# Optimization experiments

Hardware: AMD Instinct MI355X
Metric: run time of the kernel (lower is better)

The kernel has to match this reference:

```python
import jax, jax.numpy as jnp
import numpy as np

N = 100000      # nodes
E = 1600000     # edges
G = 8           # graphs in batch
H = 128         # hidden_dim
CNN = 768
MORPH = 6
NC = 5
EPS = 1e-5      # BatchNorm eps


def setup_inputs() -> dict:
    key = jax.random.key(0)
    ks = jax.random.split(key, 32)
    D = CNN + MORPH

    def w(k, shape, fan_in):
        # kaiming_normal_ (relu): std = sqrt(2/fan_in)
        return jax.random.normal(k, shape, jnp.float32) * np.sqrt(2.0 / fan_in)

    inp = {
        "cnn_features": jax.random.normal(ks[0], (N, CNN), jnp.float32),
        "morph_features": jax.random.normal(ks[1], (N, MORPH), jnp.float32),
        "cell_edge_index": jax.random.randint(ks[2], (2, E), 0, N, jnp.int32),
        "batch": jnp.sort(jax.random.randint(ks[3], (N,), 0, G, jnp.int32)),
        # GCN layers (weights stored [in, out])
        "gcn1_w": w(ks[4], (D, H), D), "gcn1_b": jnp.zeros((H,), jnp.float32),
        "gcn2_w": w(ks[5], (H, H), H), "gcn2_b": jnp.zeros((H,), jnp.float32),
        "gcn3_w": w(ks[6], (H, H), H), "gcn3_b": jnp.zeros((H,), jnp.float32),
        # BatchNorm affine params (eval mode, running_mean=0 running_var=1)
        "bn1_g": jnp.ones((H,), jnp.float32), "bn1_b": jnp.zeros((H,), jnp.float32),
        "bn2_g": jnp.ones((H,), jnp.float32), "bn2_b": jnp.zeros((H,), jnp.float32),
        "bn3_g": jnp.ones((H,), jnp.float32), "bn3_b": jnp.zeros((H,), jnp.float32),
        # attention gate: Linear(H,H) -> tanh -> Linear(H,1)
        "att_w1": w(ks[7], (H, H), H), "att_b1": jnp.zeros((H,), jnp.float32),
        "att_w2": w(ks[8], (H, 1), H), "att_b2": jnp.zeros((1,), jnp.float32),
        # classifier MLP
        "cls_w1": w(ks[9], (H, 2 * H), H), "cls_b1": jnp.zeros((2 * H,), jnp.float32),
        "cbn1_g": jnp.ones((2 * H,), jnp.float32), "cbn1_b": jnp.zeros((2 * H,), jnp.float32),
        "cls_w2": w(ks[10], (2 * H, H), 2 * H), "cls_b2": jnp.zeros((H,), jnp.float32),
        "cbn2_g": jnp.ones((H,), jnp.float32), "cbn2_b": jnp.zeros((H,), jnp.float32),
        "cls_w3": w(ks[11], (H, NC), H), "cls_b3": jnp.zeros((NC,), jnp.float32),
    }
    return inp


def _bn_eval(x, gamma, beta):
    # BatchNorm1d eval: running_mean=0, running_var=1
    return x * (gamma / np.sqrt(1.0 + EPS)) + beta


def _gcn(x, w, b, src, dst, dinv):
    h = x @ w                                   # [N, out]
    norm = dinv[src] * dinv[dst]                # [E]
    msg = h[src] * norm[:, None]                # [E, out]
    agg = jax.ops.segment_sum(msg, dst, num_segments=N)
    agg = agg + h * (dinv * dinv)[:, None]      # self-loop contribution
    return agg + b


def _forward(cnn_features, morph_features,
             gcn1_w, gcn1_b, gcn2_w, gcn2_b, gcn3_w, gcn3_b,
             bn1_g, bn1_b, bn2_g, bn2_b, bn3_g, bn3_b,
             att_w1, att_b1, att_w2, att_b2,
             cls_w1, cls_b1, cbn1_g, cbn1_b,
             cls_w2, cls_b2, cbn2_g, cbn2_b,
             cls_w3, cls_b3,
             cell_edge_index, batch):
    x = jnp.concatenate([cnn_features, morph_features], axis=1)  # [N, 774]
    src, dst = cell_edge_index[0], cell_edge_index[1]
    # symmetric GCN normalization with self-loops: deg = in-degree + 1
    deg = jax.ops.segment_sum(jnp.ones((E,), x.dtype), dst, num_segments=N) + 1.0
    dinv = jax.lax.rsqrt(deg)

    x1 = jax.nn.relu(_bn_eval(_gcn(x, gcn1_w, gcn1_b, src, dst, dinv), bn1_g, bn1_b))
    x2 = jax.nn.relu(_bn_eval(_gcn(x1, gcn2_w, gcn2_b, src, dst, dinv), bn2_g, bn2_b))
    x3 = jax.nn.relu(_bn_eval(_gcn(x2, gcn3_w, gcn3_b, src, dst, dinv), bn3_g, bn3_b))
    x_out = x1 + x2 + x3                                        # [N, H]

    # GlobalAttention pooling: segment softmax over per-graph nodes
    gate = jnp.tanh(x_out @ att_w1 + att_b1) @ att_w2 + att_b2  # [N, 1]
    gate = gate[:, 0]
    gmax = jax.ops.segment_max(gate, batch, num_segments=G)
    a = jnp.exp(gate - gmax[batch])
    denom = jax.ops.segment_sum(a, batch, num_segments=G)
    alpha = a / denom[batch]
    pooled = jax.ops.segment_sum(alpha[:, None] * x_out, batch, num_segments=G)  # [G, H]

    # classifier (dropout off, BN eval)
    h = jax.nn.relu(_bn_eval(pooled @ cls_w1 + cls_b1, cbn1_g, cbn1_b))
    h = jax.nn.relu(_bn_eval(h @ cls_w2 + cls_b2, cbn2_g, cbn2_b))
    return h @ cls_w3 + cls_b3                                  # [G, NC]


def reference(cnn_features, morph_features, cell_edge_index, batch,
              gcn1_w, gcn1_b, gcn2_w, gcn2_b, gcn3_w, gcn3_b,
              bn1_g, bn1_b, bn2_g, bn2_b, bn3_g, bn3_b,
              att_w1, att_b1, att_w2, att_b2,
              cls_w1, cls_b1, cbn1_g, cbn1_b,
              cls_w2, cls_b2, cbn2_g, cbn2_b,
              cls_w3, cls_b3):
    return _forward(cnn_features, morph_features,
                    gcn1_w, gcn1_b, gcn2_w, gcn2_b, gcn3_w, gcn3_b,
                    bn1_g, bn1_b, bn2_g, bn2_b, bn3_g, bn3_b,
                    att_w1, att_b1, att_w2, att_b2,
                    cls_w1, cls_b1, cbn1_g, cbn1_b,
                    cls_w2, cls_b2, cbn2_g, cbn2_b,
                    cls_w3, cls_b3,
                    cell_edge_index, batch)
```

## Files before the change

kernel.cpp:

```cpp
#include <hip/hip_runtime.h>
#include <hip/hip_bf16.h>

#define EPSV 1e-5f

typedef short short8v __attribute__((ext_vector_type(8)));
typedef float f32x4 __attribute__((ext_vector_type(4)));

__device__ __forceinline__ unsigned short f2bf(float f){
  unsigned u = __float_as_uint(f);
  unsigned r = u + 0x7fffu + ((u >> 16) & 1u);
  return (unsigned short)(r >> 16);
}
__device__ __forceinline__ unsigned pk2bf(float x, float y){
  return (unsigned)f2bf(x) | ((unsigned)f2bf(y) << 16);
}
__device__ __forceinline__ float bf2f(unsigned short s){
  return __uint_as_float(((unsigned)s) << 16);
}
__device__ __forceinline__ float bflo(unsigned u){ return __uint_as_float(u << 16); }
__device__ __forceinline__ float bfhi(unsigned u){ return __uint_as_float(u & 0xffff0000u); }

__global__ void hist_kernel(const int* __restrict__ dst, int* __restrict__ deg, int E){
  int i = blockIdx.x*256 + threadIdx.x;
  if (i < E) atomicAdd(&deg[dst[i]], 1);
}

__global__ void scan_partial(const int* __restrict__ deg, int* __restrict__ bsums, int N){
  __shared__ int sd[256];
  int t = threadIdx.x;
  int base = blockIdx.x*1024 + t*4;
  int s = 0;
  if (base+0 < N) s += deg[base+0];
  if (base+1 < N) s += deg[base+1];
  if (base+2 < N) s += deg[base+2];
  if (base+3 < N) s += deg[base+3];
  sd[t]=s; __syncthreads();
  for (int off=128; off>0; off>>=1){
    if (t<off) sd[t]+=sd[t+off];
    __syncthreads();
  }
  if (t==0) bsums[blockIdx.x]=sd[0];
}

__global__ void scan_bsums(int* bsums, int* row_start, int B, int N, int E){
  if (threadIdx.x==0 && blockIdx.x==0){
    int run=0;
    for (int b=0;b<B;b++){ int v=bsums[b]; bsums[b]=run; run+=v; }
    row_start[N]=E;
  }
}

__global__ void scan_final(const int* __restrict__ deg, const int* __restrict__ bsums,
                           int* __restrict__ row_start, int* __restrict__ cursor,
                           float* __restrict__ dinv, int N){
  __shared__ int sd[256];
  int t=threadIdx.x, b=blockIdx.x;
  int base=b*1024+t*4;
  int v0=0,v1=0,v2=0,v3=0;
  if (base+0<N) v0=deg[base+0];
  if (base+1<N) v1=deg[base+1];
  if (base+2<N) v2=deg[base+2];
  if (base+3<N) v3=deg[base+3];
  int s=v0+v1+v2+v3;
  sd[t]=s; __syncthreads();
  for (int off=1; off<256; off<<=1){
    int x = (t>=off)?sd[t-off]:0;
    __syncthreads();
    sd[t]+=x;
    __syncthreads();
  }
  int excl = sd[t]-s + bsums[b];
  int e0=excl, e1=excl+v0, e2=e1+v1, e3=e2+v2;
  if (base+0<N){ row_start[base+0]=e0; cursor[base+0]=e0; dinv[base+0]=rsqrtf((float)v0+1.0f); }
  if (base+1<N){ row_start[base+1]=e1; cursor[base+1]=e1; dinv[base+1]=rsqrtf((float)v1+1.0f); }
  if (base+2<N){ row_start[base+2]=e2; cursor[base+2]=e2; dinv[base+2]=rsqrtf((float)v2+1.0f); }
  if (base+3<N){ row_start[base+3]=e3; cursor[base+3]=e3; dinv[base+3]=rsqrtf((float)v3+1.0f); }
}

__global__ void scatter_kernel(const int* __restrict__ src, const int* __restrict__ dst,
                               int* __restrict__ cursor, int* __restrict__ csr_src, int E){
  int i = blockIdx.x*256 + threadIdx.x;
  if (i < E){
    int d = dst[i];
    int pos = atomicAdd(&cursor[d], 1);
    csr_src[pos] = src[i];
  }
}

__global__ void wsplit_kernel(const float* __restrict__ W, unsigned short* __restrict__ WT,
                              int D, int Dpad){
  int k = blockIdx.x*256 + threadIdx.x;
  int c = blockIdx.y;
  if (k >= Dpad) return;
  float v = (k < D) ? W[(size_t)k*128 + c] : 0.f;
  WT[(size_t)c*Dpad + k] = f2bf(v);
}

__global__ void wsplit_all(const float* __restrict__ W2, const float* __restrict__ W3,
                           const float* __restrict__ WA,
                           unsigned short* __restrict__ w2T, unsigned short* __restrict__ w3T,
                           unsigned short* __restrict__ aT_hi, unsigned short* __restrict__ aT_lo){
  int k = threadIdx.x;
  int c = blockIdx.y;
  int z = blockIdx.z;
  if (z == 0){
    w2T[c*128 + k] = f2bf(W2[(size_t)k*128 + c]);
  } else if (z == 1){
    w3T[c*128 + k] = f2bf(W3[(size_t)k*128 + c]);
  } else {
    float v = WA[(size_t)k*128 + c];
    unsigned short h = f2bf(v);
    aT_hi[c*128 + k] = h;
    aT_lo[c*128 + k] = f2bf(v - bf2f(h));
  }
}

#define LOADA(KC) { \
  const int gk0 = (KC) + akseg; \
  if ((Rst < N) && (gk0 + 32 <= Da)){ \
    const float4* p4 = (const float4*)(xa + (size_t)Rst*Da + gk0); \
    pa0=p4[0]; pa1=p4[1]; pa2=p4[2]; pa3=p4[3]; pa4=p4[4]; pa5=p4[5]; pa6=p4[6]; pa7=p4[7]; \
  } else { \
    float tmp[32]; \
    _Pragma("unroll") \
    for (int q=0;q<32;q++){ \
      int gk = gk0 + q; float x = 0.f; \
      if (Rst < N){ \
        if (gk < Da) x = xa[(size_t)Rst*Da + gk]; \
        else if (gk < D) x = xb[(size_t)Rst*Db + (gk - Da)]; \
      } \
      tmp[q]=x; } \
    pa0=*(float4*)&tmp[0];  pa1=*(float4*)&tmp[4];  pa2=*(float4*)&tmp[8];  pa3=*(float4*)&tmp[12]; \
    pa4=*(float4*)&tmp[16]; pa5=*(float4*)&tmp[20]; pa6=*(float4*)&tmp[24]; pa7=*(float4*)&tmp[28]; \
  } }

#define LOADW(KC) { \
  const unsigned short* ph = wrowp + (KC); \
  pw0=*(const uint4*)(ph); pw1=*(const uint4*)(ph+8); pw2=*(const uint4*)(ph+16); pw3=*(const uint4*)(ph+24); }

__global__ __launch_bounds__(256, 3) void gemm_mfma_kernel(
    const float* __restrict__ xa, const float* __restrict__ xb,
    const unsigned short* __restrict__ WT,
    unsigned short* __restrict__ outb, int N, int Da, int Db, int Dpad)
{
  __shared__ unsigned short Abf[128*64];
  __shared__ unsigned short Bbf[128*64];

  const int tid  = threadIdx.x;
  const int lane = tid & 63;
  const int wave = tid >> 6;
  const int lr   = lane & 15;
  const int kg   = lane >> 4;
  const int rowBase = blockIdx.x * 128;
  const int D = Da + Db;

  f32x4 acc[2][8];
  #pragma unroll
  for (int s=0;s<2;s++)
    #pragma unroll
    for (int c=0;c<8;c++){ acc[s][c][0]=0.f; acc[s][c][1]=0.f; acc[s][c][2]=0.f; acc[s][c][3]=0.f; }

  const int arow = tid >> 1;
  const int akseg = (tid & 1) * 32;
  const int Rst = rowBase + arow;
  const int abase = arow*128 + akseg*2;
  const int aswz  = (arow & 7) << 4;
  const unsigned short* wrowp = WT + (size_t)arow*Dpad + akseg;

  float4 pa0,pa1,pa2,pa3,pa4,pa5,pa6,pa7;
  uint4  pw0,pw1,pw2,pw3;

  LOADA(0)
  LOADW(0)

  for (int kc = 0; kc < Dpad; kc += 64){
    __syncthreads();
    {
      unsigned u[4];
      u[0]=pk2bf(pa0.x,pa0.y); u[1]=pk2bf(pa0.z,pa0.w); u[2]=pk2bf(pa1.x,pa1.y); u[3]=pk2bf(pa1.z,pa1.w);
      *(uint4*)((char*)Abf + ((abase+ 0)^aswz)) = *(const uint4*)u;
      u[0]=pk2bf(pa2.x,pa2.y); u[1]=pk2bf(pa2.z,pa2.w); u[2]=pk2bf(pa3.x,pa3.y); u[3]=pk2bf(pa3.z,pa3.w);
      *(uint4*)((char*)Abf + ((abase+16)^aswz)) = *(const uint4*)u;
      u[0]=pk2bf(pa4.x,pa4.y); u[1]=pk2bf(pa4.z,pa4.w); u[2]=pk2bf(pa5.x,pa5.y); u[3]=pk2bf(pa5.z,pa5.w);
      *(uint4*)((char*)Abf + ((abase+32)^aswz)) = *(const uint4*)u;
      u[0]=pk2bf(pa6.x,pa6.y); u[1]=pk2bf(pa6.z,pa6.w); u[2]=pk2bf(pa7.x,pa7.y); u[3]=pk2bf(pa7.z,pa7.w);
      *(uint4*)((char*)Abf + ((abase+48)^aswz)) = *(const uint4*)u;
      *(uint4*)((char*)Bbf + ((abase+ 0)^aswz)) = pw0;
      *(uint4*)((char*)Bbf + ((abase+16)^aswz)) = pw1;
      *(uint4*)((char*)Bbf + ((abase+32)^aswz)) = pw2;
      *(uint4*)((char*)Bbf + ((abase+48)^aswz)) = pw3;
    }
    __syncthreads();
    const int kn = kc + 64;
    if (kn < Dpad){
      LOADA(kn)
      LOADW(kn)
    }
    #pragma unroll
    for (int ks=0; ks<2; ks++){
      const int kb = ks*64 + kg*16;
      const int r0 = wave*32 + lr;
      const int r1 = r0 + 16;
      const int offA0 = (r0*128 + kb) ^ ((r0&7)<<4);
      const int offA1 = (r1*128 + kb) ^ ((r1&7)<<4);
      short8v a0 = *(const short8v*)((const char*)Abf + offA0);
      short8v a1 = *(const short8v*)((const char*)Abf + offA1);
      #pragma unroll
      for (int ct=0; ct<8; ct++){
        const int c = ct*16 + lr;
        const int offB = (c*128 + kb) ^ ((c&7)<<4);
        short8v b = *(const short8v*)((const char*)Bbf + offB);
        acc[0][ct] = __builtin_amdgcn_mfma_f32_16x16x32_bf16(a0, b, acc[0][ct], 0,0,0);
        acc[1][ct] = __builtin_amdgcn_mfma_f32_16x16x32_bf16(a1, b, acc[1][ct], 0,0,0);
      }
    }
  }
  const int wrow = rowBase + wave*32;
  #pragma unroll
  for (int strip=0; strip<2; strip++){
    #pragma unroll
    for (int ct=0; ct<8; ct++){
      #pragma unroll
      for (int i=0;i<4;i++){
        int R = wrow + strip*16 + kg*4 + i;
        int C = ct*16 + lr;
        if (R < N) outb[(size_t)R*128 + C] = f2bf(acc[strip][ct][i]);
      }
    }
  }
}

__global__ __launch_bounds__(256) void att_mfma_kernel(
    const float* __restrict__ xa,
    const unsigned short* __restrict__ WhiT, const unsigned short* __restrict__ WloT,
    const float* __restrict__ b1, const float* __restrict__ w2, const float* __restrict__ b2,
    const int* __restrict__ batch,
    float* __restrict__ aex, float* __restrict__ denom, int N)
{
  __shared__ unsigned short Ahi[128*64];
  __shared__ unsigned short Alo[128*64];
  __shared__ unsigned short Bhi[128*64];
  __shared__ unsigned short Blo[128*64];
  __shared__ float sden[8];

  const int tid  = threadIdx.x;
  const int lane = tid & 63;
  const int wave = tid >> 6;
  const int lr   = lane & 15;
  const int kg   = lane >> 4;
  const int rowBase = blockIdx.x * 128;

  if (tid < 8) sden[tid] = 0.f;

  f32x4 acc[2][8];
  #pragma unroll
  for (int s=0;s<2;s++)
    #pragma unroll
    for (int c=0;c<8;c++){ acc[s][c][0]=0.f; acc[s][c][1]=0.f; acc[s][c][2]=0.f; acc[s][c][3]=0.f; }

  const int arow = tid >> 1;
  const int akseg = (tid & 1) * 32;
  const int Rst = rowBase + arow;
  const int abase = arow*128 + akseg*2;
  const int aswz  = (arow & 7) << 4;

  for (int kc = 0; kc < 128; kc += 64){
    __syncthreads();
    {
      const int gk0 = kc + akseg;
      float4 v0={0,0,0,0},v1={0,0,0,0},v2={0,0,0,0},v3={0,0,0,0};
      float4 v4={0,0,0,0},v5={0,0,0,0},v6={0,0,0,0},v7={0,0,0,0};
      if (Rst < N){
        const float4* p4 = (const float4*)(xa + (size_t)Rst*128 + gk0);
        v0=p4[0]; v1=p4[1]; v2=p4[2]; v3=p4[3]; v4=p4[4]; v5=p4[5]; v6=p4[6]; v7=p4[7];
      }
#define STAGE_HL(VA, VB, SOFF) { \
      unsigned uh[4], ul[4]; \
      unsigned short h0=f2bf(VA.x), h1=f2bf(VA.y), h2=f2bf(VA.z), h3=f2bf(VA.w); \
      unsigned short h4=f2bf(VB.x), h5=f2bf(VB.y), h6=f2bf(VB.z), h7=f2bf(VB.w); \
      uh[0]=(unsigned)h0|((unsigned)h1<<16); uh[1]=(unsigned)h2|((unsigned)h3<<16); \
      uh[2]=(unsigned)h4|((unsigned)h5<<16); uh[3]=(unsigned)h6|((unsigned)h7<<16); \
      ul[0]=pk2bf(VA.x-bf2f(h0), VA.y-bf2f(h1)); ul[1]=pk2bf(VA.z-bf2f(h2), VA.w-bf2f(h3)); \
      ul[2]=pk2bf(VB.x-bf2f(h4), VB.y-bf2f(h5)); ul[3]=pk2bf(VB.z-bf2f(h6), VB.w-bf2f(h7)); \
      *(uint4*)((char*)Ahi + ((abase+(SOFF))^aswz)) = *(const uint4*)uh; \
      *(uint4*)((char*)Alo + ((abase+(SOFF))^aswz)) = *(const uint4*)ul; }
      STAGE_HL(v0, v1,  0)
      STAGE_HL(v2, v3, 16)
      STAGE_HL(v4, v5, 32)
      STAGE_HL(v6, v7, 48)
#undef STAGE_HL
    }
    {
      const unsigned short* ph = WhiT + (size_t)arow*128 + kc + akseg;
      const unsigned short* pl = WloT + (size_t)arow*128 + kc + akseg;
      *(uint4*)((char*)Bhi + ((abase+ 0)^aswz)) = *(const uint4*)(ph);
      *(uint4*)((char*)Bhi + ((abase+16)^aswz)) = *(const uint4*)(ph+8);
      *(uint4*)((char*)Bhi + ((abase+32)^aswz)) = *(const uint4*)(ph+16);
      *(uint4*)((char*)Bhi + ((abase+48)^aswz)) = *(const uint4*)(ph+24);
      *(uint4*)((char*)Blo + ((abase+ 0)^aswz)) = *(const uint4*)(pl);
      *(uint4*)((char*)Blo + ((abase+16)^aswz)) = *(const uint4*)(pl+8);
      *(uint4*)((char*)Blo + ((abase+32)^aswz)) = *(const uint4*)(pl+16);
      *(uint4*)((char*)Blo + ((abase+48)^aswz)) = *(const uint4*)(pl+24);
    }
    __syncthreads();
    #pragma unroll
    for (int ks=0; ks<2; ks++){
      const int kb = ks*64 + kg*16;
      const int r0 = wave*32 + lr;
      const int r1 = r0 + 16;
      const int offA0 = (r0*128 + kb) ^ ((r0&7)<<4);
      const int offA1 = (r1*128 + kb) ^ ((r1&7)<<4);
      short8v ah0 = *(const short8v*)((const char*)Ahi + offA0);
      short8v al0 = *(const short8v*)((const char*)Alo + offA0);
      short8v ah1 = *(const short8v*)((const char*)Ahi + offA1);
      short8v al1 = *(const short8v*)((const char*)Alo + offA1);
      #pragma unroll
      for (int ct=0; ct<8; ct++){
        const int c = ct*16 + lr;
        const int offB = (c*128 + kb) ^ ((c&7)<<4);
        short8v bh = *(const short8v*)((const char*)Bhi + offB);
        short8v bl = *(const short8v*)((const char*)Blo + offB);
        acc[0][ct] = __builtin_amdgcn_mfma_f32_16x16x32_bf16(ah0, bh, acc[0][ct], 0,0,0);
        acc[0][ct] = __builtin_amdgcn_mfma_f32_16x16x32_bf16(ah0, bl, acc[0][ct], 0,0,0);
        acc[0][ct] = __builtin_amdgcn_mfma_f32_16x16x32_bf16(al0, bh, acc[0][ct], 0,0,0);
        acc[1][ct] = __builtin_amdgcn_mfma_f32_16x16x32_bf16(ah1, bh, acc[1][ct], 0,0,0);
        acc[1][ct] = __builtin_amdgcn_mfma_f32_16x16x32_bf16(ah1, bl, acc[1][ct], 0,0,0);
        acc[1][ct] = __builtin_amdgcn_mfma_f32_16x16x32_bf16(al1, bh, acc[1][ct], 0,0,0);
      }
    }
  }
  float b1v[8], w2v[8];
  #pragma unroll
  for (int ct=0; ct<8; ct++){
    b1v[ct] = b1[ct*16 + lr];
    w2v[ct] = w2[ct*16 + lr];
  }
  const float bias2 = b2[0];
  const int wrow = rowBase + wave*32;
  #pragma unroll
  for (int strip=0; strip<2; strip++){
    #pragma unroll
    for (int i=0;i<4;i++){
      float p = 0.f;
      #pragma unroll
      for (int ct=0; ct<8; ct++){
        p += tanhf(acc[strip][ct][i] + b1v[ct]) * w2v[ct];
      }
      p += __shfl_xor(p, 1, 16);
      p += __shfl_xor(p, 2, 16);
      p += __shfl_xor(p, 4, 16);
      p += __shfl_xor(p, 8, 16);
      if (lr == 0){
        int R = wrow + strip*16 + kg*4 + i;
        if (R < N){
          float e = expf(p + bias2);
          aex[R] = e;
          atomicAdd(&sden[batch[R]], e);
        }
      }
    }
  }
  __syncthreads();
  if (tid < 8 && sden[tid] != 0.f) atomicAdd(&denom[tid], sden[tid]);
}

#define GFMA8(U, NJ) \
  a0=__builtin_fmaf(bflo(U.x),(NJ),a0); a1=__builtin_fmaf(bfhi(U.x),(NJ),a1); \
  a2=__builtin_fmaf(bflo(U.y),(NJ),a2); a3=__builtin_fmaf(bfhi(U.y),(NJ),a3); \
  a4=__builtin_fmaf(bflo(U.z),(NJ),a4); a5=__builtin_fmaf(bfhi(U.z),(NJ),a5); \
  a6=__builtin_fmaf(bflo(U.w),(NJ),a6); a7=__builtin_fmaf(bfhi(U.w),(NJ),a7);

__global__ __launch_bounds__(256) void gather_kernel(
    const unsigned short* __restrict__ hb, const float* __restrict__ dinv,
    const int* __restrict__ row_start, const int* __restrict__ csr_src,
    const float* __restrict__ bias, const float* __restrict__ bng, const float* __restrict__ bnb,
    const float* __restrict__ x1in, const float* __restrict__ x2in,
    float* __restrict__ out, int N, int mode)
{
  const int grp = (blockIdx.x * 256 + threadIdx.x) >> 4;
  const int sl  = threadIdx.x & 15;
  if (grp >= N) return;
  const int i = grp;
  const float di = dinv[i];
  const uint4* __restrict__ h4 = (const uint4*)hb;

  float a0,a1,a2,a3,a4,a5,a6,a7;
  {
    uint4 u = h4[(size_t)i*16 + sl];
    float w0 = di*di;
    a0=bflo(u.x)*w0; a1=bfhi(u.x)*w0; a2=bflo(u.y)*w0; a3=bfhi(u.y)*w0;
    a4=bflo(u.z)*w0; a5=bfhi(u.z)*w0; a6=bflo(u.w)*w0; a7=bfhi(u.w)*w0;
  }
  int base = row_start[i];
  const int s1 = row_start[i+1];
  while (base + 16 <= s1){
    int sv = csr_src[base + sl];
    float nv = dinv[sv]*di;
    #pragma unroll
    for (int j=0; j<16; j+=4){
      int sj0 = __shfl(sv, j,   16);
      int sj1 = __shfl(sv, j+1, 16);
      int sj2 = __shfl(sv, j+2, 16);
      int sj3 = __shfl(sv, j+3, 16);
      float nj0 = __shfl(nv, j,   16);
      float nj1 = __shfl(nv, j+1, 16);
      float nj2 = __shfl(nv, j+2, 16);
      float nj3 = __shfl(nv, j+3, 16);
      uint4 u0 = h4[(size_t)sj0*16 + sl];
      uint4 u1 = h4[(size_t)sj1*16 + sl];
      uint4 u2 = h4[(size_t)sj2*16 + sl];
      uint4 u3 = h4[(size_t)sj3*16 + sl];
      GFMA8(u0, nj0)
      GFMA8(u1, nj1)
      GFMA8(u2, nj2)
      GFMA8(u3, nj3)
    }
    base += 16;
  }
  const int rem = s1 - base;
  if (rem > 0){
    int sv = 0; float nv = 0.f;
    if (sl < rem){ sv = csr_src[base + sl]; nv = dinv[sv]*di; }
    for (int j=0; j<rem; j++){
      int   sj = __shfl(sv, j, 16);
      float nj = __shfl(nv, j, 16);
      uint4 u = h4[(size_t)sj*16 + sl];
      GFMA8(u, nj)
    }
  }
  const int f0 = sl*8;
  const float bsc = rsqrtf(1.0f + EPSV);
  float4 bi0 = *(const float4*)(bias + f0);
  float4 bi1 = *(const float4*)(bias + f0 + 4);
  float4 g0 = *(const float4*)(bng + f0);
  float4 g1 = *(const float4*)(bng + f0 + 4);
  float4 be0 = *(const float4*)(bnb + f0);
  float4 be1 = *(const float4*)(bnb + f0 + 4);
  float v[8];
  v[0] = fmaxf(0.f, (a0+bi0.x)*(g0.x*bsc) + be0.x);
  v[1] = fmaxf(0.f, (a1+bi0.y)*(g0.y*bsc) + be0.y);
  v[2] = fmaxf(0.f, (a2+bi0.z)*(g0.z*bsc) + be0.z);
  v[3] = fmaxf(0.f, (a3+bi0.w)*(g0.w*bsc) + be0.w);
  v[4] = fmaxf(0.f, (a4+bi1.x)*(g1.x*bsc) + be1.x);
  v[5] = fmaxf(0.f, (a5+bi1.y)*(g1.y*bsc) + be1.y);
  v[6] = fmaxf(0.f, (a6+bi1.z)*(g1.z*bsc) + be1.z);
  v[7] = fmaxf(0.f, (a7+bi1.w)*(g1.w*bsc) + be1.w);
  if (mode == 2){
    float4 p0 = *(const float4*)(x1in + (size_t)i*128 + f0);
    float4 p1 = *(const float4*)(x1in + (size_t)i*128 + f0 + 4);
    float4 q0 = *(const float4*)(x2in + (size_t)i*128 + f0);
    float4 q1 = *(const float4*)(x2in + (size_t)i*128 + f0 + 4);
    v[0]+=p0.x+q0.x; v[1]+=p0.y+q0.y; v[2]+=p0.z+q0.z; v[3]+=p0.w+q0.w;
    v[4]+=p1.x+q1.x; v[5]+=p1.y+q1.y; v[6]+=p1.z+q1.z; v[7]+=p1.w+q1.w;
  }
  float4 o0; o0.x=v[0]; o0.y=v[1]; o0.z=v[2]; o0.w=v[3];
  float4 o1; o1.x=v[4]; o1.y=v[5]; o1.z=v[6]; o1.w=v[7];
  *(float4*)(out + (size_t)i*128 + f0)     = o0;
  *(float4*)(out + (size_t)i*128 + f0 + 4) = o1;
}

__global__ void pooled_kernel(const float* __restrict__ aex, const float* __restrict__ xo,
                              const int* __restrict__ batch, float* __restrict__ pooled, int N){
  int t = threadIdx.x;
  int hlf = t >> 7;
  int f = t & 127;
  int nb = gridDim.x;
  int per = (N + nb - 1)/nb;
  int start = blockIdx.x*per;
  int end = (N < start + per) ? N : (start + per);
  float acc = 0.f; int gcur = -1;
  for (int i = start + hlf; i < end; i += 2){
    int g = batch[i];
    if (g != gcur){
      if (gcur >= 0) atomicAdd(&pooled[gcur*128 + f], acc);
      acc = 0.f; gcur = g;
    }
    acc = __builtin_fmaf(aex[i], xo[(size_t)i*128 + f], acc);
  }
  if (gcur >= 0) atomicAdd(&pooled[gcur*128 + f], acc);
}

__global__ __launch_bounds__(256) void classifier_kernel(
    const float* __restrict__ pooled, const float* __restrict__ denom,
    const float* __restrict__ w1, const float* __restrict__ b1,
    const float* __restrict__ g1, const float* __restrict__ be1,
    const float* __restrict__ w2, const float* __restrict__ b2,
    const float* __restrict__ g2, const float* __restrict__ be2,
    const float* __restrict__ w3, const float* __restrict__ b3,
    float* __restrict__ outp)
{
  __shared__ float pl[8*128];
  __shared__ float h1[8*256];
  __shared__ float h2l[8*128];
  int t = threadIdx.x;
  for (int idx = t; idx < 1024; idx += 256){
    int g = idx >> 7;
    pl[idx] = pooled[idx] / denom[g];
  }
  __syncthreads();
  {
    float a0=0,a1=0,a2=0,a3=0,a4=0,a5=0,a6=0,a7=0;
    for (int k=0; k<128; k++){
      float w = w1[k*256 + t];
      a0 = __builtin_fmaf(pl[0*128+k], w, a0);
      a1 = __builtin_fmaf(pl[1*128+k], w, a1);
      a2 = __builtin_fmaf(pl[2*128+k], w, a2);
      a3 = __builtin_fmaf(pl[3*128+k], w, a3);
      a4 = __builtin_fmaf(pl[4*128+k], w, a4);
      a5 = __builtin_fmaf(pl[5*128+k], w, a5);
      a6 = __builtin_fmaf(pl[6*128+k], w, a6);
      a7 = __builtin_fmaf(pl[7*128+k], w, a7);
    }
    float s = g1[t]*rsqrtf(1.0f + EPSV);
    float bb = b1[t], tb = be1[t];
    h1[0*256+t] = fmaxf(0.f, (a0+bb)*s + tb);
    h1[1*256+t] = fmaxf(0.f, (a1+bb)*s + tb);
    h1[2*256+t] = fmaxf(0.f, (a2+bb)*s + tb);
    h1[3*256+t] = fmaxf(0.f, (a3+bb)*s + tb);
    h1[4*256+t] = fmaxf(0.f, (a4+bb)*s + tb);
    h1[5*256+t] = fmaxf(0.f, (a5+bb)*s + tb);
    h1[6*256+t] = fmaxf(0.f, (a6+bb)*s + tb);
    h1[7*256+t] = fmaxf(0.f, (a7+bb)*s + tb);
  }
  __syncthreads();
  if (t < 128){
    float a0=0,a1=0,a2=0,a3=0,a4=0,a5=0,a6=0,a7=0;
    for (int k=0; k<256; k++){
      float w = w2[k*128 + t];
      a0 = __builtin_fmaf(h1[0*256+k], w, a0);
      a1 = __builtin_fmaf(h1[1*256+k], w, a1);
      a2 = __builtin_fmaf(h1[2*256+k], w, a2);
      a3 = __builtin_fmaf(h1[3*256+k], w, a3);
      a4 = __builtin_fmaf(h1[4*256+k], w, a4);
      a5 = __builtin_fmaf(h1[5*256+k], w, a5);
      a6 = __builtin_fmaf(h1[6*256+k], w, a6);
      a7 = __builtin_fmaf(h1[7*256+k], w, a7);
    }
    float s = g2[t]*rsqrtf(1.0f + EPSV);
    float bb = b2[t], tb = be2[t];
    h2l[0*128+t] = fmaxf(0.f, (a0+bb)*s + tb);
    h2l[1*128+t] = fmaxf(0.f, (a1+bb)*s + tb);
    h2l[2*128+t] = fmaxf(0.f, (a2+bb)*s + tb);
    h2l[3*128+t] = fmaxf(0.f, (a3+bb)*s + tb);
    h2l[4*128+t] = fmaxf(0.f, (a4+bb)*s + tb);
    h2l[5*128+t] = fmaxf(0.f, (a5+bb)*s + tb);
    h2l[6*128+t] = fmaxf(0.f, (a6+bb)*s + tb);
    h2l[7*128+t] = fmaxf(0.f, (a7+bb)*s + tb);
  }
  __syncthreads();
  if (t < 40){
    int g = t/5, c = t%5;
    float s = 0.f;
    for (int k=0; k<128; k++) s = __builtin_fmaf(h2l[g*128+k], w3[k*5+c], s);
    outp[t] = s + b3[c];
  }
}

extern "C" void kernel_launch(void* const* d_in, const int* in_sizes, int n_in,
                              void* d_out, int out_size, void* d_ws, size_t ws_size,
                              hipStream_t stream)
{
  const float* cnn   = (const float*)d_in[0];
  const float* morph = (const float*)d_in[1];
  const int*   eidx  = (const int*)d_in[2];
  const int*   batch = (const int*)d_in[3];
  const float* g1w = (const float*)d_in[4];
  const float* g1b = (const float*)d_in[5];
  const float* g2w = (const float*)d_in[6];
  const float* g2b = (const float*)d_in[7];
  const float* g3w = (const float*)d_in[8];
  const float* g3b = (const float*)d_in[9];
  const float* bn1g=(const float*)d_in[10], *bn1b=(const float*)d_in[11];
  const float* bn2g=(const float*)d_in[12], *bn2b=(const float*)d_in[13];
  const float* bn3g=(const float*)d_in[14], *bn3b=(const float*)d_in[15];
  const float* aw1=(const float*)d_in[16], *ab1=(const float*)d_in[17];
  const float* aw2=(const float*)d_in[18], *ab2=(const float*)d_in[19];
  const float* cw1=(const float*)d_in[20], *cb1=(const float*)d_in[21];
  const float* c1g=(const float*)d_in[22], *c1b=(const float*)d_in[23];
  const float* cw2=(const float*)d_in[24], *cb2=(const float*)d_in[25];
  const float* c2g=(const float*)d_in[26], *c2b=(const float*)d_in[27];
  const float* cw3=(const float*)d_in[28], *cb3=(const float*)d_in[29];

  const int N = in_sizes[3];
  const int E = in_sizes[2] / 2;
  const int CNNW = in_sizes[0] / N;
  const int MOR  = in_sizes[1] / N;
  const int D = CNNW + MOR;
  const int Dpad1 = ((D + 63)/64)*64;

  char* p = (char*)d_ws;
  auto alloc = [&](size_t bytes)->char* {
    char* r = p; p += (bytes + 255) & ~(size_t)255; return r;
  };
  unsigned short* hbuf = (unsigned short*)alloc((size_t)N*128*2);
  float* x1    = (float*)alloc((size_t)N*128*4);
  float* x2    = (float*)alloc((size_t)N*128*4);
  float* dinv  = (float*)alloc((size_t)N*4);
  float* aex   = (float*)alloc((size_t)N*4);
  char* zstart = p;
  int* deg      = (int*)alloc((size_t)N*4);
  float* denom  = (float*)alloc(8*4);
  float* pooled = (float*)alloc(8*128*4);
  size_t zbytes = (size_t)(p - zstart);
  int* row_start=(int*)alloc((size_t)(N+1)*4);
  int* cursor  = (int*)alloc((size_t)N*4);
  int* csr_src = (int*)alloc((size_t)E*4);
  int* bsums   = (int*)alloc(4096);
  unsigned short* w1T = (unsigned short*)alloc((size_t)128*Dpad1*2);
  unsigned short* w2T = (unsigned short*)alloc((size_t)128*128*2);
  unsigned short* w3T = (unsigned short*)alloc((size_t)128*128*2);
  unsigned short* aw1hiT = (unsigned short*)alloc((size_t)128*128*2);
  unsigned short* aw1loT = (unsigned short*)alloc((size_t)128*128*2);

  hipMemsetAsync(zstart, 0, zbytes, stream);

  const int* srcp = eidx;
  const int* dstp = eidx + E;

  int gE = (E + 255)/256;
  int B  = (N + 1023)/1024;
  int gMfma = (N + 127)/128;
  int gGat  = (N + 15)/16;

  hist_kernel<<<dim3(gE), dim3(256), 0, stream>>>(dstp, deg, E);
  scan_partial<<<dim3(B), dim3(256), 0, stream>>>(deg, bsums, N);
  scan_bsums<<<dim3(1), dim3(64), 0, stream>>>(bsums, row_start, B, N, E);
  scan_final<<<dim3(B), dim3(256), 0, stream>>>(deg, bsums, row_start, cursor, dinv, N);
  scatter_kernel<<<dim3(gE), dim3(256), 0, stream>>>(srcp, dstp, cursor, csr_src, E);

  wsplit_kernel<<<dim3((Dpad1+255)/256, 128), dim3(256), 0, stream>>>(g1w, w1T, D, Dpad1);
  wsplit_all<<<dim3(1, 128, 3), dim3(128), 0, stream>>>(g2w, g3w, aw1, w2T, w3T, aw1hiT, aw1loT);

  gemm_mfma_kernel<<<dim3(gMfma), dim3(256), 0, stream>>>(cnn, morph, w1T, hbuf, N, CNNW, MOR, Dpad1);
  gather_kernel<<<dim3(gGat), dim3(256), 0, stream>>>(hbuf, dinv, row_start, csr_src,
      g1b, bn1g, bn1b, (const float*)nullptr, (const float*)nullptr, x1, N, 0);
  gemm_mfma_kernel<<<dim3(gMfma), dim3(256), 0, stream>>>(x1, (const float*)nullptr, w2T, hbuf, N, 128, 0, 128);
  gather_kernel<<<dim3(gGat), dim3(256), 0, stream>>>(hbuf, dinv, row_start, csr_src,
      g2b, bn2g, bn2b, (const float*)nullptr, (const float*)nullptr, x2, N, 0);
  gemm_mfma_kernel<<<dim3(gMfma), dim3(256), 0, stream>>>(x2, (const float*)nullptr, w3T, hbuf, N, 128, 0, 128);
  gather_kernel<<<dim3(gGat), dim3(256), 0, stream>>>(hbuf, dinv, row_start, csr_src,
      g3b, bn3g, bn3b, x1, x2, x1, N, 2);

  att_mfma_kernel<<<dim3(gMfma), dim3(256), 0, stream>>>(x1, aw1hiT, aw1loT,
      ab1, aw2, ab2, batch, aex, denom, N);
  pooled_kernel<<<dim3(512), dim3(256), 0, stream>>>(aex, x1, batch, pooled, N);

  classifier_kernel<<<dim3(1), dim3(256), 0, stream>>>(pooled, denom,
      cw1, cb1, c1g, c1b, cw2, cb2, c2g, c2b, cw3, cb3, (float*)d_out);
}
```

Measured before the change: 751.3 us.

## Store intermediate activations in bf16 and fuse attention pooling into attention kernel

Intermediate node features x1/x2 are now stored as bf16 instead of fp32, which halves their memory traffic. A dedicated bf16 GEMM kernel loads them directly and prefetches the next K chunk, with no fp32-to-bf16 conversion inside the kernel. The attention kernel drops the A-side hi/lo split, so it issues two MFMAs per tile instead of three. It also fuses the attention-weighted pooling, keeping the per-row exp values in shared memory and removing both the aex buffer and the separate pooled kernel. The cost is lower precision in the stored activations and in the residual sum.

```diff
diff --git a/kernel.cpp b/kernel.cpp
--- a/kernel.cpp
+++ b/kernel.cpp
@@ -230,18 +230,13 @@
   }
 }
 
-__global__ __launch_bounds__(256) void att_mfma_kernel(
-    const float* __restrict__ xa,
-    const unsigned short* __restrict__ WhiT, const unsigned short* __restrict__ WloT,
-    const float* __restrict__ b1, const float* __restrict__ w2, const float* __restrict__ b2,
-    const int* __restrict__ batch,
-    float* __restrict__ aex, float* __restrict__ denom, int N)
+__global__ __launch_bounds__(256, 3) void gemm_bf16_kernel(
+    const unsigned short* __restrict__ xa,
+    const unsigned short* __restrict__ WT,
+    unsigned short* __restrict__ outb, int N)
 {
-  __shared__ unsigned short Ahi[128*64];
-  __shared__ unsigned short Alo[128*64];
-  __shared__ unsigned short Bhi[128*64];
-  __shared__ unsigned short Blo[128*64];
-  __shared__ float sden[8];
+  __shared__ unsigned short Abf[128*64];
+  __shared__ unsigned short Bbf[128*64];
 
   const int tid  = threadIdx.x;
   const int lane = tid & 63;
@@ -250,8 +245,6 @@
   const int kg   = lane >> 4;
   const int rowBase = blockIdx.x * 128;
 
-  if (tid < 8) sden[tid] = 0.f;
-
   f32x4 acc[2][8];
   #pragma unroll
   for (int s=0;s<2;s++)
@@ -263,34 +256,119 @@
   const int Rst = rowBase + arow;
   const int abase = arow*128 + akseg*2;
   const int aswz  = (arow & 7) << 4;
-
+  const unsigned short* arp = xa + (size_t)Rst*128 + akseg;
+  const unsigned short* wrp = WT + (size_t)arow*128 + akseg;
+
+  uint4 pa0,pa1,pa2,pa3, pw0,pw1,pw2,pw3;
+  uint4 z4; z4.x=0; z4.y=0; z4.z=0; z4.w=0;
+  if (Rst < N){ pa0=*(const uint4*)(arp); pa1=*(const uint4*)(arp+8); pa2=*(const uint4*)(arp+16); pa3=*(const uint4*)(arp+24); }
+  else { pa0=z4; pa1=z4; pa2=z4; pa3=z4; }
+  pw0=*(const uint4*)(wrp); pw1=*(const uint4*)(wrp+8); pw2=*(const uint4*)(wrp+16); pw3=*(const uint4*)(wrp+24);
+
+  #pragma unroll
   for (int kc = 0; kc < 128; kc += 64){
     __syncthreads();
+    *(uint4*)((char*)Abf + ((abase+ 0)^aswz)) = pa0;
+    *(uint4*)((char*)Abf + ((abase+16)^aswz)) = pa1;
+    *(uint4*)((char*)Abf + ((abase+32)^aswz)) = pa2;
+    *(uint4*)((char*)Abf + ((abase+48)^aswz)) = pa3;
+    *(uint4*)((char*)Bbf + ((abase+ 0)^aswz)) = pw0;
+    *(uint4*)((char*)Bbf + ((abase+16)^aswz)) = pw1;
+    *(uint4*)((char*)Bbf + ((abase+32)^aswz)) = pw2;
+    *(uint4*)((char*)Bbf + ((abase+48)^aswz)) = pw3;
+    __syncthreads();
+    if (kc == 0){
+      if (Rst < N){ pa0=*(const uint4*)(arp+64); pa1=*(const uint4*)(arp+72); pa2=*(const uint4*)(arp+80); pa3=*(const uint4*)(arp+88); }
+      pw0=*(const uint4*)(wrp+64); pw1=*(const uint4*)(wrp+72); pw2=*(const uint4*)(wrp+80); pw3=*(const uint4*)(wrp+88);
+    }
+    #pragma unroll
+    for (int ks=0; ks<2; ks++){
+      const int kb = ks*64 + kg*16;
+      const int r0 = wave*32 + lr;
+      const int r1 = r0 + 16;
+      const int offA0 = (r0*128 + kb) ^ ((r0&7)<<4);
+      const int offA1 = (r1*128 + kb) ^ ((r1&7)<<4);
+      short8v a0 = *(const short8v*)((const char*)Abf + offA0);
+      short8v a1 = *(const short8v*)((const char*)Abf + offA1);
+      #pragma unroll
+      for (int ct=0; ct<8; ct++){
+        const int c = ct*16 + lr;
+        const int offB = (c*128 + kb) ^ ((c&7)<<4);
+        short8v b = *(const short8v*)((const char*)Bbf + offB);
+        acc[0][ct] = __builtin_amdgcn_mfma_f32_16x16x32_bf16(a0, b, acc[0][ct], 0,0,0);
+        acc[1][ct] = __builtin_amdgcn_mfma_f32_16x16x32_bf16(a1, b, acc[1][ct], 0,0,0);
+      }
+    }
+  }
+  const int wrow = rowBase + wave*32;
+  #pragma unroll
+  for (int strip=0; strip<2; strip++){
+    #pragma unroll
+    for (int ct=0; ct<8; ct++){
+      #pragma unroll
+      for (int i=0;i<4;i++){
+        int R = wrow + strip*16 + kg*4 + i;
+        int C = ct*16 + lr;
+        if (R < N) outb[(size_t)R*128 + C] = f2bf(acc[strip][ct][i]);
+      }
+    }
+  }
+}
+
+__global__ __launch_bounds__(256) void att_pool_kernel(
+    const unsigned short* __restrict__ xa,
+    const unsigned short* __restrict__ WhiT, const unsigned short* __restrict__ WloT,
+    const float* __restrict__ b1, const float* __restrict__ w2, const float* __restrict__ b2,
+    const int* __restrict__ batch,
+    float* __restrict__ pooled, float* __restrict__ denom, int N)
+{
+  __shared__ unsigned short Abf[128*64];
+  __shared__ unsigned short Bhi[128*64];
+  __shared__ unsigned short Blo[128*64];
+  __shared__ float sden[8];
+  __shared__ float sAex[128];
+  __shared__ int   sBatch[128];
+
+  const int tid  = threadIdx.x;
+  const int lane = tid & 63;
+  const int wave = tid >> 6;
+  const int lr   = lane & 15;
+  const int kg   = lane >> 4;
+  const int rowBase = blockIdx.x * 128;
+
+  if (tid < 8) sden[tid] = 0.f;
+  if (tid < 128){
+    int R = rowBase + tid;
+    sBatch[tid] = (R < N) ? batch[R] : -1;
+  }
+
+  f32x4 acc[2][8];
+  #pragma unroll
+  for (int s=0;s<2;s++)
+    #pragma unroll
+    for (int c=0;c<8;c++){ acc[s][c][0]=0.f; acc[s][c][1]=0.f; acc[s][c][2]=0.f; acc[s][c][3]=0.f; }
+
+  const int arow = tid >> 1;
+  const int akseg = (tid & 1) * 32;
+  const int Rst = rowBase + arow;
+  const int abase = arow*128 + akseg*2;
+  const int aswz  = (arow & 7) << 4;
+  const unsigned short* arp = xa + (size_t)Rst*128 + akseg;
+
+  #pragma unroll
+  for (int kc = 0; kc < 128; kc += 64){
+    __syncthreads();
     {
-      const int gk0 = kc + akseg;
-      float4 v0={0,0,0,0},v1={0,0,0,0},v2={0,0,0,0},v3={0,0,0,0};
-      float4 v4={0,0,0,0},v5={0,0,0,0},v6={0,0,0,0},v7={0,0,0,0};
+      uint4 z4; z4.x=0; z4.y=0; z4.z=0; z4.w=0;
+      uint4 a0=z4,a1=z4,a2=z4,a3=z4;
       if (Rst < N){
-        const float4* p4 = (const float4*)(xa + (size_t)Rst*128 + gk0);
-        v0=p4[0]; v1=p4[1]; v2=p4[2]; v3=p4[3]; v4=p4[4]; v5=p4[5]; v6=p4[6]; v7=p4[7];
-      }
-#define STAGE_HL(VA, VB, SOFF) { \
-      unsigned uh[4], ul[4]; \
-      unsigned short h0=f2bf(VA.x), h1=f2bf(VA.y), h2=f2bf(VA.z), h3=f2bf(VA.w); \
-      unsigned short h4=f2bf(VB.x), h5=f2bf(VB.y), h6=f2bf(VB.z), h7=f2bf(VB.w); \
-      uh[0]=(unsigned)h0|((unsigned)h1<<16); uh[1]=(unsigned)h2|((unsigned)h3<<16); \
-      uh[2]=(unsigned)h4|((unsigned)h5<<16); uh[3]=(unsigned)h6|((unsigned)h7<<16); \
-      ul[0]=pk2bf(VA.x-bf2f(h0), VA.y-bf2f(h1)); ul[1]=pk2bf(VA.z-bf2f(h2), VA.w-bf2f(h3)); \
-      ul[2]=pk2bf(VB.x-bf2f(h4), VB.y-bf2f(h5)); ul[3]=pk2bf(VB.z-bf2f(h6), VB.w-bf2f(h7)); \
-      *(uint4*)((char*)Ahi + ((abase+(SOFF))^aswz)) = *(const uint4*)uh; \
-      *(uint4*)((char*)Alo + ((abase+(SOFF))^aswz)) = *(const uint4*)ul; }
-      STAGE_HL(v0, v1,  0)
-      STAGE_HL(v2, v3, 16)
-      STAGE_HL(v4, v5, 32)
-      STAGE_HL(v6, v7, 48)
-#undef STAGE_HL
-    }
-    {
+        a0=*(const uint4*)(arp+kc); a1=*(const uint4*)(arp+kc+8);
+        a2=*(const uint4*)(arp+kc+16); a3=*(const uint4*)(arp+kc+24);
+      }
+      *(uint4*)((char*)Abf + ((abase+ 0)^aswz)) = a0;
+      *(uint4*)((char*)Abf + ((abase+16)^aswz)) = a1;
+      *(uint4*)((char*)Abf + ((abase+32)^aswz)) = a2;
+      *(uint4*)((char*)Abf + ((abase+48)^aswz)) = a3;
       const unsigned short* ph = WhiT + (size_t)arow*128 + kc + akseg;
       const unsigned short* pl = WloT + (size_t)arow*128 + kc + akseg;
       *(uint4*)((char*)Bhi + ((abase+ 0)^aswz)) = *(const uint4*)(ph);
@@ -310,22 +388,18 @@
       const int r1 = r0 + 16;
       const int offA0 = (r0*128 + kb) ^ ((r0&7)<<4);
       const int offA1 = (r1*128 + kb) ^ ((r1&7)<<4);
-      short8v ah0 = *(const short8v*)((const char*)Ahi + offA0);
-      short8v al0 = *(const short8v*)((const char*)Alo + offA0);
-      short8v ah1 = *(const short8v*)((const char*)Ahi + offA1);
-      short8v al1 = *(const short8v*)((const char*)Alo + offA1);
+      short8v a0 = *(const short8v*)((const char*)Abf + offA0);
+      short8v a1 = *(const short8v*)((const char*)Abf + offA1);
       #pragma unroll
       for (int ct=0; ct<8; ct++){
         const int c = ct*16 + lr;
         const int offB = (c*128 + kb) ^ ((c&7)<<4);
         short8v bh = *(const short8v*)((const char*)Bhi + offB);
         short8v bl = *(const short8v*)((const char*)Blo + offB);
-        acc[0][ct] = __builtin_amdgcn_mfma_f32_16x16x32_bf16(ah0, bh, acc[0][ct], 0,0,0);
-        acc[0][ct] = __builtin_amdgcn_mfma_f32_16x16x32_bf16(ah0, bl, acc[0][ct], 0,0,0);
-        acc[0][ct] = __builtin_amdgcn_mfma_f32_16x16x32_bf16(al0, bh, acc[0][ct], 0,0,0);
-        acc[1][ct] = __builtin_amdgcn_mfma_f32_16x16x32_bf16(ah1, bh, acc[1][ct], 0,0,0);
-        acc[1][ct] = __builtin_amdgcn_mfma_f32_16x16x32_bf16(ah1, bl, acc[1][ct], 0,0,0);
-        acc[1][ct] = __builtin_amdgcn_mfma_f32_16x16x32_bf16(al1, bh, acc[1][ct], 0,0,0);
+        acc[0][ct] = __builtin_amdgcn_mfma_f32_16x16x32_bf16(a0, bh, acc[0][ct], 0,0,0);
+        acc[0][ct] = __builtin_amdgcn_mfma_f32_16x16x32_bf16(a0, bl, acc[0][ct], 0,0,0);
+        acc[1][ct] = __builtin_amdgcn_mfma_f32_16x16x32_bf16(a1, bh, acc[1][ct], 0,0,0);
+        acc[1][ct] = __builtin_amdgcn_mfma_f32_16x16x32_bf16(a1, bl, acc[1][ct], 0,0,0);
       }
     }
   }
@@ -336,7 +410,6 @@
     w2v[ct] = w2[ct*16 + lr];
   }
   const float bias2 = b2[0];
-  const int wrow = rowBase + wave*32;
   #pragma unroll
   for (int strip=0; strip<2; strip++){
     #pragma unroll
@@ -351,16 +424,44 @@
       p += __shfl_xor(p, 4, 16);
       p += __shfl_xor(p, 8, 16);
       if (lr == 0){
-        int R = wrow + strip*16 + kg*4 + i;
+        int rib = wave*32 + strip*16 + kg*4 + i;
+        int R = rowBase + rib;
         if (R < N){
           float e = expf(p + bias2);
-          aex[R] = e;
-          atomicAdd(&sden[batch[R]], e);
+          sAex[rib] = e;
+          atomicAdd(&sden[sBatch[rib]], e);
         }
       }
     }
   }
   __syncthreads();
+  {
+    const int cpair = tid & 63;
+    const int rgrp  = tid >> 6;
+    const unsigned* __restrict__ xu = (const unsigned*)xa;
+    float p0 = 0.f, p1 = 0.f;
+    int gcur = -1;
+    for (int r = rgrp*32; r < rgrp*32 + 32; ++r){
+      int R = rowBase + r;
+      if (R >= N) break;
+      int g = sBatch[r];
+      if (g != gcur){
+        if (gcur >= 0){
+          atomicAdd(&pooled[gcur*128 + cpair*2],     p0);
+          atomicAdd(&pooled[gcur*128 + cpair*2 + 1], p1);
+        }
+        p0 = 0.f; p1 = 0.f; gcur = g;
+      }
+      float e = sAex[r];
+      unsigned u = xu[(size_t)R*64 + cpair];
+      p0 = __builtin_fmaf(e, bflo(u), p0);
+      p1 = __builtin_fmaf(e, bfhi(u), p1);
+    }
+    if (gcur >= 0){
+      atomicAdd(&pooled[gcur*128 + cpair*2],     p0);
+      atomicAdd(&pooled[gcur*128 + cpair*2 + 1], p1);
+    }
+  }
   if (tid < 8 && sden[tid] != 0.f) atomicAdd(&denom[tid], sden[tid]);
 }
 
@@ -374,8 +475,8 @@
     const unsigned short* __restrict__ hb, const float* __restrict__ dinv,
     const int* __restrict__ row_start, const int* __restrict__ csr_src,
     const float* __restrict__ bias, const float* __restrict__ bng, const float* __restrict__ bnb,
-    const float* __restrict__ x1in, const float* __restrict__ x2in,
-    float* __restrict__ out, int N, int mode)
+    const unsigned short* __restrict__ x1in, const unsigned short* __restrict__ x2in,
+    unsigned short* __restrict__ out, int N, int mode)
 {
   const int grp = (blockIdx.x * 256 + threadIdx.x) >> 4;
   const int sl  = threadIdx.x & 15;
@@ -446,38 +547,16 @@
   v[6] = fmaxf(0.f, (a6+bi1.z)*(g1.z*bsc) + be1.z);
   v[7] = fmaxf(0.f, (a7+bi1.w)*(g1.w*bsc) + be1.w);
   if (mode == 2){
-    float4 p0 = *(const float4*)(x1in + (size_t)i*128 + f0);
-    float4 p1 = *(const float4*)(x1in + (size_t)i*128 + f0 + 4);
-    float4 q0 = *(const float4*)(x2in + (size_t)i*128 + f0);
-    float4 q1 = *(const float4*)(x2in + (size_t)i*128 + f0 + 4);
-    v[0]+=p0.x+q0.x; v[1]+=p0.y+q0.y; v[2]+=p0.z+q0.z; v[3]+=p0.w+q0.w;
-    v[4]+=p1.x+q1.x; v[5]+=p1.y+q1.y; v[6]+=p1.z+q1.z; v[7]+=p1.w+q1.w;
-  }
-  float4 o0; o0.x=v[0]; o0.y=v[1]; o0.z=v[2]; o0.w=v[3];
-  float4 o1; o1.x=v[4]; o1.y=v[5]; o1.z=v[6]; o1.w=v[7];
-  *(float4*)(out + (size_t)i*128 + f0)     = o0;
-  *(float4*)(out + (size_t)i*128 + f0 + 4) = o1;
-}
-
-__global__ void pooled_kernel(const float* __restrict__ aex, const float* __restrict__ xo,
-                              const int* __restrict__ batch, float* __restrict__ pooled, int N){
-  int t = threadIdx.x;
-  int hlf = t >> 7;
-  int f = t & 127;
-  int nb = gridDim.x;
-  int per = (N + nb - 1)/nb;
-  int start = blockIdx.x*per;
-  int end = (N < start + per) ? N : (start + per);
-  float acc = 0.f; int gcur = -1;
-  for (int i = start + hlf; i < end; i += 2){
-    int g = batch[i];
-    if (g != gcur){
-      if (gcur >= 0) atomicAdd(&pooled[gcur*128 + f], acc);
-      acc = 0.f; gcur = g;
-    }
-    acc = __builtin_fmaf(aex[i], xo[(size_t)i*128 + f], acc);
-  }
-  if (gcur >= 0) atomicAdd(&pooled[gcur*128 + f], acc);
+    uint4 up = ((const uint4*)x1in)[(size_t)i*16 + sl];
+    uint4 uq = ((const uint4*)x2in)[(size_t)i*16 + sl];
+    v[0]+=bflo(up.x)+bflo(uq.x); v[1]+=bfhi(up.x)+bfhi(uq.x);
+    v[2]+=bflo(up.y)+bflo(uq.y); v[3]+=bfhi(up.y)+bfhi(uq.y);
+    v[4]+=bflo(up.z)+bflo(uq.z); v[5]+=bfhi(up.z)+bfhi(uq.z);
+    v[6]+=bflo(up.w)+bflo(uq.w); v[7]+=bfhi(up.w)+bfhi(uq.w);
+  }
+  unsigned o[4];
+  o[0]=pk2bf(v[0],v[1]); o[1]=pk2bf(v[2],v[3]); o[2]=pk2bf(v[4],v[5]); o[3]=pk2bf(v[6],v[7]);
+  ((uint4*)out)[(size_t)i*16 + sl] = *(const uint4*)o;
 }
 
 __global__ __launch_bounds__(256) void classifier_kernel(
@@ -593,10 +672,9 @@
     char* r = p; p += (bytes + 255) & ~(size_t)255; return r;
   };
   unsigned short* hbuf = (unsigned short*)alloc((size_t)N*128*2);
-  float* x1    = (float*)alloc((size_t)N*128*4);
-  float* x2    = (float*)alloc((size_t)N*128*4);
+  unsigned short* x1   = (unsigned short*)alloc((size_t)N*128*2);
+  unsigned short* x2   = (unsigned short*)alloc((size_t)N*128*2);
   float* dinv  = (float*)alloc((size_t)N*4);
-  float* aex   = (float*)alloc((size_t)N*4);
   char* zstart = p;
   int* deg      = (int*)alloc((size_t)N*4);
   float* denom  = (float*)alloc(8*4);
@@ -633,17 +711,16 @@
 
   gemm_mfma_kernel<<<dim3(gMfma), dim3(256), 0, stream>>>(cnn, morph, w1T, hbuf, N, CNNW, MOR, Dpad1);
   gather_kernel<<<dim3(gGat), dim3(256), 0, stream>>>(hbuf, dinv, row_start, csr_src,
-      g1b, bn1g, bn1b, (const float*)nullptr, (const float*)nullptr, x1, N, 0);
-  gemm_mfma_kernel<<<dim3(gMfma), dim3(256), 0, stream>>>(x1, (const float*)nullptr, w2T, hbuf, N, 128, 0, 128);
+      g1b, bn1g, bn1b, (const unsigned short*)nullptr, (const unsigned short*)nullptr, x1, N, 0);
+  gemm_bf16_kernel<<<dim3(gMfma), dim3(256), 0, stream>>>(x1, w2T, hbuf, N);
   gather_kernel<<<dim3(gGat), dim3(256), 0, stream>>>(hbuf, dinv, row_start, csr_src,
-      g2b, bn2g, bn2b, (const float*)nullptr, (const float*)nullptr, x2, N, 0);
-  gemm_mfma_kernel<<<dim3(gMfma), dim3(256), 0, stream>>>(x2, (const float*)nullptr, w3T, hbuf, N, 128, 0, 128);
+      g2b, bn2g, bn2b, (const unsigned short*)nullptr, (const unsigned short*)nullptr, x2, N, 0);
+  gemm_bf16_kernel<<<dim3(gMfma), dim3(256), 0, stream>>>(x2, w3T, hbuf, N);
   gather_kernel<<<dim3(gGat), dim3(256), 0, stream>>>(hbuf, dinv, row_start, csr_src,
       g3b, bn3g, bn3b, x1, x2, x1, N, 2);
 
-  att_mfma_kernel<<<dim3(gMfma), dim3(256), 0, stream>>>(x1, aw1hiT, aw1loT,
-      ab1, aw2, ab2, batch, aex, denom, N);
-  pooled_kernel<<<dim3(512), dim3(256), 0, stream>>>(aex, x1, batch, pooled, N);
+  att_pool_kernel<<<dim3(gMfma), dim3(256), 0, stream>>>(x1, aw1hiT, aw1loT,
+      ab1, aw2, ab2, batch, pooled, denom, N);
 
   classifier_kernel<<<dim3(1), dim3(256), 0, stream>>>(pooled, denom,
       cw1, cb1, c1g, c1b, cw2, cb2, c2g, c2b, cw3, cb3, (float*)d_out);
```

New measurement: 725.8 us. 1.04x faster.
